# Optimization experiments

Measured on AMD Instinct MI355X. Metric: run time of the kernel, lower is better.

Reference implementation:

```python
import jax, jax.numpy as jnp
import numpy as np

EPS = 1e-6

def feature_map(x):
    # 'elu' feature map: elu(x) + 1 (positive feature map from Katharopoulos et al.)
    return jax.nn.elu(x) + 1.0

def setup_inputs() -> dict:
    key = jax.random.key(0)
    kq, kk, kv = jax.random.split(key, 3)
    B, L, H, D = 4, 2048, 16, 64
    q = jax.random.normal(kq, (B, L, H, D), dtype=jnp.float32)
    k = jax.random.normal(kk, (B, L, H, D), dtype=jnp.float32)
    v = jax.random.normal(kv, (B, L, H, D), dtype=jnp.float32)
    return {"q": q, "k": k, "v": v}

def reference(q, k, v):
    # q, k, v: [N, L, H, D]  (attention_mask=None -> causal linear attention)
    qf = feature_map(q)
    kf = feature_map(k)
    # normalizer: z[n,l,h] = sum_d qf[n,l,h,d] * cumsum_s<=l kf[n,s,h,d]
    z = jnp.einsum('nlhd,nlhd->nlh', qf, jnp.cumsum(kf, axis=1)) + EPS
    # causal_dot_product via scan over sequence with carry S[n,h,d,m]
    B, L, H, D = q.shape
    M = v.shape[-1]
    qs = jnp.moveaxis(qf, 1, 0)  # [L, N, H, D]
    ks = jnp.moveaxis(kf, 1, 0)
    vs = jnp.moveaxis(v, 1, 0)

    def step(S, qkv):
        ql, kl, vl = qkv                              # [N,H,D], [N,H,D], [N,H,M]
        S = S + jnp.einsum('nhd,nhm->nhdm', kl, vl)   # running sum of k v^T
        out = jnp.einsum('nhd,nhdm->nhm', ql, S)
        return S, out

    S0 = jnp.zeros((B, H, D, M), dtype=q.dtype)
    _, outs = jax.lax.scan(step, S0, (qs, ks, vs))    # outs: [L, N, H, M]
    v_ = jnp.moveaxis(outs, 0, 1)                     # [N, L, H, M]
    return v_ / z[..., None]
```

## Files before the change

### kernel.cpp

```cpp
#include <hip/hip_runtime.h>
#include <cstdint>

#define LL 2048
#define HH 16
#define DD 64
#define NC 32
#define LSTR 1024
#define EPSF 1e-6f
#define PAD 72

typedef __bf16 bf16x8 __attribute__((ext_vector_type(8)));
typedef float floatx4 __attribute__((ext_vector_type(4)));
typedef unsigned short ushortx8 __attribute__((ext_vector_type(8)));
typedef unsigned short ushortx4 __attribute__((ext_vector_type(4)));
typedef unsigned short ushortx2 __attribute__((ext_vector_type(2)));

static __device__ __forceinline__ float fmap(float x){ return x > 0.f ? x + 1.f : __expf(x); }
static __device__ __forceinline__ unsigned short f2bf(float f){
    unsigned u = __builtin_bit_cast(unsigned, f);
    u += 0x7fffu + ((u >> 16) & 1u);
    return (unsigned short)(u >> 16);
}
static __device__ __forceinline__ float bf2f(unsigned short s){
    unsigned u = ((unsigned)s) << 16;
    return __builtin_bit_cast(float, u);
}
static __device__ __forceinline__ bf16x8 ldf(const unsigned short* p){
    return __builtin_bit_cast(bf16x8, *(const ushortx8*)p);
}

__global__ __launch_bounds__(256) void k1(const float* __restrict__ kp, const float* __restrict__ vp,
                                          unsigned short* __restrict__ kvt, float* __restrict__ ks)
{
    __shared__ __align__(16) unsigned short kft[DD*PAD];
    __shared__ __align__(16) unsigned short vtt[DD*PAD];
    const int ci = blockIdx.x;
    const int c = ci & 31, bh = ci >> 5, b = bh >> 4, h = bh & 15;
    const int t = threadIdx.x;
    const int64_t gbase = ((int64_t)(b*LL + c*DD)*HH + h)*DD;
#pragma unroll
    for (int i = 0; i < 2; ++i) {
        int flat = t + 256*i;
        int l0 = (flat >> 4) * 2, col = (flat & 15) << 2;
        const float* gk = kp + gbase + (int64_t)l0*LSTR + col;
        const float* gv = vp + gbase + (int64_t)l0*LSTR + col;
        float4 ka = *(const float4*)(gk);
        float4 kb = *(const float4*)(gk + LSTR);
        float4 va = *(const float4*)(gv);
        float4 vb = *(const float4*)(gv + LSTR);
        float kaa[4] = {ka.x,ka.y,ka.z,ka.w}, kbb[4] = {kb.x,kb.y,kb.z,kb.w};
        float vaa[4] = {va.x,va.y,va.z,va.w}, vbb[4] = {vb.x,vb.y,vb.z,vb.w};
#pragma unroll
        for (int e = 0; e < 4; ++e) {
            *(ushortx2*)(kft + (col+e)*PAD + l0) = ushortx2{ f2bf(fmap(kaa[e])), f2bf(fmap(kbb[e])) };
            *(ushortx2*)(vtt + (col+e)*PAD + l0) = ushortx2{ f2bf(vaa[e]), f2bf(vbb[e]) };
        }
    }
    __syncthreads();
    const int w = t >> 6, lane = t & 63, quad = lane >> 4, lr = lane & 15;
    const int m0 = 16*w;
    floatx4 acc[4];
#pragma unroll
    for (int dt = 0; dt < 4; ++dt) acc[dt] = floatx4{0.f,0.f,0.f,0.f};
#pragma unroll
    for (int kk = 0; kk < 2; ++kk) {
        bf16x8 a = ldf(vtt + (m0+lr)*PAD + kk*32 + quad*8);
#pragma unroll
        for (int dt = 0; dt < 4; ++dt) {
            bf16x8 bb = ldf(kft + (dt*16+lr)*PAD + kk*32 + quad*8);
            acc[dt] = __builtin_amdgcn_mfma_f32_16x16x32_bf16(a, bb, acc[dt], 0, 0, 0);
        }
    }
    unsigned short* kvo = kvt + (int64_t)ci*4096;
#pragma unroll
    for (int dt = 0; dt < 4; ++dt)
#pragma unroll
        for (int r = 0; r < 4; ++r)
            kvo[(m0 + quad*4 + r)*DD + dt*16 + lr] = f2bf(acc[dt][r]);
    if (t < DD) {
        float s = 0.f;
#pragma unroll
        for (int j = 0; j < 8; ++j) {
            ushortx8 u = *(const ushortx8*)(kft + t*PAD + j*8);
#pragma unroll
            for (int e = 0; e < 8; ++e) s += bf2f(u[e]);
        }
        ks[(int64_t)ci*DD + t] = s;
    }
}

__global__ __launch_bounds__(256) void k2(unsigned short* __restrict__ kvt, float* __restrict__ ks)
{
    const int blk = blockIdx.x;
    const int bh = blk >> 3, part = blk & 7, t = threadIdx.x;
    unsigned short* base = kvt + (int64_t)bh*NC*4096 + (part*256 + t)*2;
    float r0 = 0.f, r1 = 0.f;
    unsigned x = *(const unsigned*)base;
    for (int c = 0; c < NC-1; ++c) {
        unsigned xn = *(const unsigned*)(base + (int64_t)(c+1)*4096);
        unsigned o = (unsigned)f2bf(r0) | ((unsigned)f2bf(r1) << 16);
        r0 += bf2f((unsigned short)(x & 0xffffu));
        r1 += bf2f((unsigned short)(x >> 16));
        *(unsigned*)(base + (int64_t)c*4096) = o;
        x = xn;
    }
    *(unsigned*)(base + (int64_t)(NC-1)*4096) = (unsigned)f2bf(r0) | ((unsigned)f2bf(r1) << 16);
    if (part == 0 && t < DD) {
        float r = 0.f;
        float* kb = ks + (int64_t)bh*NC*DD + t;
        for (int c = 0; c < NC; ++c) { float xx = kb[(int64_t)c*DD]; kb[(int64_t)c*DD] = r; r += xx; }
    }
}

__global__ __launch_bounds__(256) void k3(const float* __restrict__ qp, const float* __restrict__ kp,
                                          const float* __restrict__ vp,
                                          const unsigned short* __restrict__ kvt,
                                          const float* __restrict__ ks, float* __restrict__ outp)
{
    __shared__ __align__(16) unsigned short qf [DD*PAD];
    __shared__ __align__(16) unsigned short kfx[80*PAD];
    __shared__ __align__(16) unsigned short vtt[DD*PAD];
    __shared__ float zr[DD];
    const int ci = blockIdx.x;
    const int c = ci & 31, bh = ci >> 5, b = bh >> 4, h = bh & 15;
    const int t = threadIdx.x;
    const int64_t gbase = ((int64_t)(b*LL + c*DD)*HH + h)*DD;
    const unsigned short* kvg = kvt + (int64_t)ci*4096;
    const float* ksg = ks + (int64_t)ci*DD;
#pragma unroll
    for (int i = 0; i < 2; ++i) {
        int flat = t + 256*i;
        int l0 = (flat >> 4) * 2, col = (flat & 15) << 2;
        const float* gq = qp + gbase + (int64_t)l0*LSTR + col;
        const float* gk = kp + gbase + (int64_t)l0*LSTR + col;
        const float* gv = vp + gbase + (int64_t)l0*LSTR + col;
        float4 qa = *(const float4*)(gq);
        float4 qb = *(const float4*)(gq + LSTR);
        float4 ka = *(const float4*)(gk);
        float4 kb = *(const float4*)(gk + LSTR);
        float4 va = *(const float4*)(gv);
        float4 vb = *(const float4*)(gv + LSTR);
        *(ushortx4*)(qf + l0*PAD + col)      = ushortx4{ f2bf(fmap(qa.x)), f2bf(fmap(qa.y)), f2bf(fmap(qa.z)), f2bf(fmap(qa.w)) };
        *(ushortx4*)(qf + (l0+1)*PAD + col)  = ushortx4{ f2bf(fmap(qb.x)), f2bf(fmap(qb.y)), f2bf(fmap(qb.z)), f2bf(fmap(qb.w)) };
        *(ushortx4*)(kfx + l0*PAD + col)     = ushortx4{ f2bf(fmap(ka.x)), f2bf(fmap(ka.y)), f2bf(fmap(ka.z)), f2bf(fmap(ka.w)) };
        *(ushortx4*)(kfx + (l0+1)*PAD + col) = ushortx4{ f2bf(fmap(kb.x)), f2bf(fmap(kb.y)), f2bf(fmap(kb.z)), f2bf(fmap(kb.w)) };
        float vaa[4] = {va.x,va.y,va.z,va.w}, vbb[4] = {vb.x,vb.y,vb.z,vb.w};
#pragma unroll
        for (int e = 0; e < 4; ++e)
            *(ushortx2*)(vtt + (col+e)*PAD + l0) = ushortx2{ f2bf(vaa[e]), f2bf(vbb[e]) };
    }
    if (t < 135) *(ushortx8*)(kfx + 65*PAD + t*8) = ushortx8{0,0,0,0,0,0,0,0};
    if (t < DD)  kfx[64*PAD + t] = f2bf(ksg[t]);
    __syncthreads();

    const int w = t >> 6, lane = t & 63, quad = lane >> 4, lr = lane & 15;
    const int l0 = 16*w;
    bf16x8 aq[2];
    aq[0] = ldf(qf + (l0+lr)*PAD + quad*8);
    aq[1] = ldf(qf + (l0+lr)*PAD + 32 + quad*8);
    bf16x8 bs[2][4];
#pragma unroll
    for (int kk = 0; kk < 2; ++kk)
#pragma unroll
        for (int mt = 0; mt < 4; ++mt)
            bs[kk][mt] = ldf(kvg + (mt*16+lr)*DD + kk*32 + quad*8);

    floatx4 sc[5];
#pragma unroll
    for (int tt = 0; tt < 5; ++tt) sc[tt] = floatx4{0.f,0.f,0.f,0.f};
#pragma unroll
    for (int kk = 0; kk < 2; ++kk)
#pragma unroll
        for (int tt = 0; tt < 5; ++tt) {
            bf16x8 bb = ldf(kfx + (tt*16+lr)*PAD + kk*32 + quad*8);
            sc[tt] = __builtin_amdgcn_mfma_f32_16x16x32_bf16(aq[kk], bb, sc[tt], 0, 0, 0);
        }

    float zp[4] = {0.f,0.f,0.f,0.f};
#pragma unroll
    for (int tt = 0; tt < 4; ++tt)
#pragma unroll
        for (int r = 0; r < 4; ++r) {
            int row = l0 + quad*4 + r;
            int col = tt*16 + lr;
            float val = (col <= row) ? sc[tt][r] : 0.f;
            zp[r] += val;
            qf[row*PAD + col] = f2bf(val);
        }
#pragma unroll
    for (int r = 0; r < 4; ++r) zp[r] += (lr == 0) ? sc[4][r] : 0.f;
#pragma unroll
    for (int m = 1; m < 16; m <<= 1)
#pragma unroll
        for (int r = 0; r < 4; ++r) zp[r] += __shfl_xor(zp[r], m, 64);
    if (lr == 0)
#pragma unroll
        for (int r = 0; r < 4; ++r) zr[l0 + quad*4 + r] = 1.f / (zp[r] + EPSF);

    floatx4 oa[4];
#pragma unroll
    for (int mt = 0; mt < 4; ++mt) oa[mt] = floatx4{0.f,0.f,0.f,0.f};
#pragma unroll
    for (int kk = 0; kk < 2; ++kk) {
        bf16x8 a2 = ldf(qf + (l0+lr)*PAD + kk*32 + quad*8);
#pragma unroll
        for (int mt = 0; mt < 4; ++mt) {
            bf16x8 bv = ldf(vtt + (mt*16+lr)*PAD + kk*32 + quad*8);
            oa[mt] = __builtin_amdgcn_mfma_f32_16x16x32_bf16(a2, bv, oa[mt], 0, 0, 0);
        }
    }
#pragma unroll
    for (int kk = 0; kk < 2; ++kk)
#pragma unroll
        for (int mt = 0; mt < 4; ++mt)
            oa[mt] = __builtin_amdgcn_mfma_f32_16x16x32_bf16(aq[kk], bs[kk][mt], oa[mt], 0, 0, 0);
#pragma unroll
    for (int r = 0; r < 4; ++r) {
        int row = l0 + quad*4 + r;
        float rz = zr[row];
#pragma unroll
        for (int mt = 0; mt < 4; ++mt)
            outp[gbase + (int64_t)row*LSTR + mt*16 + lr] = oa[mt][r] * rz;
    }
}

extern "C" void kernel_launch(void* const* d_in, const int* in_sizes, int n_in,
                              void* d_out, int out_size, void* d_ws, size_t ws_size,
                              hipStream_t stream) {
    const float* q = (const float*)d_in[0];
    const float* k = (const float*)d_in[1];
    const float* v = (const float*)d_in[2];
    float* out = (float*)d_out;
    unsigned short* kvt = (unsigned short*)d_ws;
    float* ks = (float*)((char*)d_ws + (size_t)2048*4096*2);
    k1<<<2048, 256, 0, stream>>>(k, v, kvt, ks);
    k2<<<512,  256, 0, stream>>>(kvt, ks);
    k3<<<2048, 256, 0, stream>>>(q, k, v, kvt, ks, out);
}
```

Before: 156.3 us.

## Restructure into two kernels with per-quarter serial state recurrence

Replaces the three-kernel chunked scheme (per-chunk KV, global prefix scan, output) with two kernels. The first computes KV sums over 256-row octets, double-buffering global loads into LDS. The second has each 512-thread block own a quarter of one (b,h) sequence, seed its state from the preceding octet sums, and walk 8 chunks serially, updating the running KV state and key sum in LDS while prefetching the next chunk. This removes the bf16 scan kernel and a workspace round trip. In exchange the main kernel launches only 256 blocks and has a serial chunk dependency, so parallelism drops.

Result: faster. 147.8 us (-5.5%).

```diff
diff --git a/kernel.cpp b/kernel.cpp
--- a/kernel.cpp
+++ b/kernel.cpp
@@ -4,7 +4,6 @@
 #define LL 2048
 #define HH 16
 #define DD 64
-#define NC 32
 #define LSTR 1024
 #define EPSF 1e-6f
 #define PAD 72
@@ -28,199 +27,301 @@
 static __device__ __forceinline__ bf16x8 ldf(const unsigned short* p){
     return __builtin_bit_cast(bf16x8, *(const ushortx8*)p);
 }
-
-__global__ __launch_bounds__(256) void k1(const float* __restrict__ kp, const float* __restrict__ vp,
-                                          unsigned short* __restrict__ kvt, float* __restrict__ ks)
+static __device__ __forceinline__ float4 fmap4(float4 a){
+    return float4{fmap(a.x), fmap(a.y), fmap(a.z), fmap(a.w)};
+}
+
+template<bool MAP>
+static __device__ __forceinline__ void st_sd(unsigned short* base, int r, int c, float4 a, float4 b){
+    if (MAP) {
+        *(ushortx4*)(base + r*PAD + c)     = ushortx4{ f2bf(fmap(a.x)), f2bf(fmap(a.y)), f2bf(fmap(a.z)), f2bf(fmap(a.w)) };
+        *(ushortx4*)(base + (r+1)*PAD + c) = ushortx4{ f2bf(fmap(b.x)), f2bf(fmap(b.y)), f2bf(fmap(b.z)), f2bf(fmap(b.w)) };
+    } else {
+        *(ushortx4*)(base + r*PAD + c)     = ushortx4{ f2bf(a.x), f2bf(a.y), f2bf(a.z), f2bf(a.w) };
+        *(ushortx4*)(base + (r+1)*PAD + c) = ushortx4{ f2bf(b.x), f2bf(b.y), f2bf(b.z), f2bf(b.w) };
+    }
+}
+template<bool MAP>
+static __device__ __forceinline__ void st_tr(unsigned short* base, int r, int c, float4 a, float4 b){
+    float aa[4] = {a.x, a.y, a.z, a.w}, bb[4] = {b.x, b.y, b.z, b.w};
+#pragma unroll
+    for (int e = 0; e < 4; ++e) {
+        float x0 = MAP ? fmap(aa[e]) : aa[e];
+        float x1 = MAP ? fmap(bb[e]) : bb[e];
+        *(ushortx2*)(base + (c+e)*PAD + r) = ushortx2{ f2bf(x0), f2bf(x1) };
+    }
+}
+
+__global__ __launch_bounds__(256) void kA(const float* __restrict__ kp, const float* __restrict__ vp,
+                                          float* __restrict__ qkv, float* __restrict__ ksq)
 {
+    __shared__ __align__(16) unsigned short kft[2][DD*PAD];
+    __shared__ __align__(16) unsigned short vtt[2][DD*PAD];
+    const int blk = blockIdx.x;
+    const int bh = blk >> 3, oct = blk & 7, b = bh >> 4, h = bh & 15;
+    const int t = threadIdx.x;
+    const int w = t >> 6, lane = t & 63, quad = lane >> 4, lr = lane & 15;
+    const int m0 = 16*w;
+
+    floatx4 acc[4];
+#pragma unroll
+    for (int dt = 0; dt < 4; ++dt) acc[dt] = floatx4{0.f,0.f,0.f,0.f};
+    float ksa = 0.f;
+
+    const int64_t gb0 = ((int64_t)(b*LL + oct*256)*HH + h)*DD;
+#pragma unroll
+    for (int ii = 0; ii < 2; ++ii) {
+        int flat = t + 256*ii;
+        int l0s = (flat >> 4) * 2, col4 = (flat & 15) << 2;
+        const float* gk = kp + gb0 + (int64_t)l0s*LSTR + col4;
+        const float* gv = vp + gb0 + (int64_t)l0s*LSTR + col4;
+        float4 ka = *(const float4*)gk, kb = *(const float4*)(gk + LSTR);
+        float4 va = *(const float4*)gv, vb = *(const float4*)(gv + LSTR);
+        st_tr<true >(kft[0], l0s, col4, ka, kb);
+        st_tr<false>(vtt[0], l0s, col4, va, vb);
+    }
+    __syncthreads();
+
+#pragma unroll
+    for (int sc = 0; sc < 4; ++sc) {
+        const int p = sc & 1;
+        float4 ka[2], kb[2], va[2], vb[2];
+        if (sc < 3) {
+            const int64_t gb = gb0 + (int64_t)(sc+1)*DD*LSTR;
+#pragma unroll
+            for (int ii = 0; ii < 2; ++ii) {
+                int flat = t + 256*ii;
+                int l0s = (flat >> 4) * 2, col4 = (flat & 15) << 2;
+                const float* gk = kp + gb + (int64_t)l0s*LSTR + col4;
+                const float* gv = vp + gb + (int64_t)l0s*LSTR + col4;
+                ka[ii] = *(const float4*)gk; kb[ii] = *(const float4*)(gk + LSTR);
+                va[ii] = *(const float4*)gv; vb[ii] = *(const float4*)(gv + LSTR);
+            }
+        }
+#pragma unroll
+        for (int kk = 0; kk < 2; ++kk) {
+            bf16x8 a = ldf(vtt[p] + (m0+lr)*PAD + kk*32 + quad*8);
+#pragma unroll
+            for (int dt = 0; dt < 4; ++dt) {
+                bf16x8 bbf = ldf(kft[p] + (dt*16+lr)*PAD + kk*32 + quad*8);
+                acc[dt] = __builtin_amdgcn_mfma_f32_16x16x32_bf16(a, bbf, acc[dt], 0, 0, 0);
+            }
+        }
+        if (t < DD) {
+#pragma unroll
+            for (int jj = 0; jj < 8; ++jj) {
+                ushortx8 u = *(const ushortx8*)(kft[p] + t*PAD + jj*8);
+#pragma unroll
+                for (int e = 0; e < 8; ++e) ksa += bf2f(u[e]);
+            }
+        }
+        if (sc < 3) {
+#pragma unroll
+            for (int ii = 0; ii < 2; ++ii) {
+                int flat = t + 256*ii;
+                int l0s = (flat >> 4) * 2, col4 = (flat & 15) << 2;
+                st_tr<true >(kft[p^1], l0s, col4, ka[ii], kb[ii]);
+                st_tr<false>(vtt[p^1], l0s, col4, va[ii], vb[ii]);
+            }
+        }
+        __syncthreads();
+    }
+
+    float* qo = qkv + (int64_t)blk*4096;
+#pragma unroll
+    for (int dt = 0; dt < 4; ++dt)
+#pragma unroll
+        for (int r = 0; r < 4; ++r)
+            qo[(m0 + quad*4 + r)*DD + dt*16 + lr] = acc[dt][r];
+    if (t < DD) ksq[(int64_t)blk*DD + t] = ksa;
+}
+
+__global__ __launch_bounds__(512) void kM(const float* __restrict__ qp, const float* __restrict__ kp,
+                                          const float* __restrict__ vp,
+                                          const float* __restrict__ qkv, const float* __restrict__ ksq,
+                                          float* __restrict__ outp)
+{
+    __shared__ __align__(16) unsigned short qf [DD*PAD];
+    __shared__ __align__(16) unsigned short kfx[DD*PAD];
     __shared__ __align__(16) unsigned short kft[DD*PAD];
     __shared__ __align__(16) unsigned short vtt[DD*PAD];
-    const int ci = blockIdx.x;
-    const int c = ci & 31, bh = ci >> 5, b = bh >> 4, h = bh & 15;
+    __shared__ __align__(16) unsigned short sld[DD*PAD];
+    __shared__ __align__(16) unsigned short sct[DD*PAD];
+    __shared__ __align__(16) unsigned short kpx[16*PAD];
+    __shared__ float ksum[DD];
+    __shared__ float zp2[2][DD];
+
+    const int bid = blockIdx.x;
+    const int bh = bid & 63, qtr = bid >> 6, b = bh >> 4, h = bh & 15;
     const int t = threadIdx.x;
-    const int64_t gbase = ((int64_t)(b*LL + c*DD)*HH + h)*DD;
-#pragma unroll
-    for (int i = 0; i < 2; ++i) {
-        int flat = t + 256*i;
-        int l0 = (flat >> 4) * 2, col = (flat & 15) << 2;
-        const float* gk = kp + gbase + (int64_t)l0*LSTR + col;
-        const float* gv = vp + gbase + (int64_t)l0*LSTR + col;
-        float4 ka = *(const float4*)(gk);
-        float4 kb = *(const float4*)(gk + LSTR);
-        float4 va = *(const float4*)(gv);
-        float4 vb = *(const float4*)(gv + LSTR);
-        float kaa[4] = {ka.x,ka.y,ka.z,ka.w}, kbb[4] = {kb.x,kb.y,kb.z,kb.w};
-        float vaa[4] = {va.x,va.y,va.z,va.w}, vbb[4] = {vb.x,vb.y,vb.z,vb.w};
-#pragma unroll
-        for (int e = 0; e < 4; ++e) {
-            *(ushortx2*)(kft + (col+e)*PAD + l0) = ushortx2{ f2bf(fmap(kaa[e])), f2bf(fmap(kbb[e])) };
-            *(ushortx2*)(vtt + (col+e)*PAD + l0) = ushortx2{ f2bf(vaa[e]), f2bf(vbb[e]) };
-        }
-    }
-    __syncthreads();
     const int w = t >> 6, lane = t & 63, quad = lane >> 4, lr = lane & 15;
-    const int m0 = 16*w;
-    floatx4 acc[4];
-#pragma unroll
-    for (int dt = 0; dt < 4; ++dt) acc[dt] = floatx4{0.f,0.f,0.f,0.f};
-#pragma unroll
-    for (int kk = 0; kk < 2; ++kk) {
-        bf16x8 a = ldf(vtt + (m0+lr)*PAD + kk*32 + quad*8);
-#pragma unroll
-        for (int dt = 0; dt < 4; ++dt) {
-            bf16x8 bb = ldf(kft + (dt*16+lr)*PAD + kk*32 + quad*8);
-            acc[dt] = __builtin_amdgcn_mfma_f32_16x16x32_bf16(a, bb, acc[dt], 0, 0, 0);
-        }
-    }
-    unsigned short* kvo = kvt + (int64_t)ci*4096;
-#pragma unroll
-    for (int dt = 0; dt < 4; ++dt)
-#pragma unroll
-        for (int r = 0; r < 4; ++r)
-            kvo[(m0 + quad*4 + r)*DD + dt*16 + lr] = f2bf(acc[dt][r]);
+    const int wi = w >> 1, wj = w & 1;
+    const int l0 = 16*wi;
+    const int l0s = (t >> 4) * 2, col4 = (t & 15) << 2;
+
+    const int64_t bhb = ((int64_t)b*LL*HH + h)*DD;
+    const int cg0 = qtr*8;
+
+    if (t < 135) *(ushortx8*)(kpx + PAD + t*8) = ushortx8{0,0,0,0,0,0,0,0};
+    const int no = 2*qtr;
     if (t < DD) {
         float s = 0.f;
-#pragma unroll
-        for (int j = 0; j < 8; ++j) {
-            ushortx8 u = *(const ushortx8*)(kft + t*PAD + j*8);
-#pragma unroll
-            for (int e = 0; e < 8; ++e) s += bf2f(u[e]);
-        }
-        ks[(int64_t)ci*DD + t] = s;
-    }
-}
-
-__global__ __launch_bounds__(256) void k2(unsigned short* __restrict__ kvt, float* __restrict__ ks)
-{
-    const int blk = blockIdx.x;
-    const int bh = blk >> 3, part = blk & 7, t = threadIdx.x;
-    unsigned short* base = kvt + (int64_t)bh*NC*4096 + (part*256 + t)*2;
-    float r0 = 0.f, r1 = 0.f;
-    unsigned x = *(const unsigned*)base;
-    for (int c = 0; c < NC-1; ++c) {
-        unsigned xn = *(const unsigned*)(base + (int64_t)(c+1)*4096);
-        unsigned o = (unsigned)f2bf(r0) | ((unsigned)f2bf(r1) << 16);
-        r0 += bf2f((unsigned short)(x & 0xffffu));
-        r1 += bf2f((unsigned short)(x >> 16));
-        *(unsigned*)(base + (int64_t)c*4096) = o;
-        x = xn;
-    }
-    *(unsigned*)(base + (int64_t)(NC-1)*4096) = (unsigned)f2bf(r0) | ((unsigned)f2bf(r1) << 16);
-    if (part == 0 && t < DD) {
-        float r = 0.f;
-        float* kb = ks + (int64_t)bh*NC*DD + t;
-        for (int c = 0; c < NC; ++c) { float xx = kb[(int64_t)c*DD]; kb[(int64_t)c*DD] = r; r += xx; }
-    }
-}
-
-__global__ __launch_bounds__(256) void k3(const float* __restrict__ qp, const float* __restrict__ kp,
-                                          const float* __restrict__ vp,
-                                          const unsigned short* __restrict__ kvt,
-                                          const float* __restrict__ ks, float* __restrict__ outp)
-{
-    __shared__ __align__(16) unsigned short qf [DD*PAD];
-    __shared__ __align__(16) unsigned short kfx[80*PAD];
-    __shared__ __align__(16) unsigned short vtt[DD*PAD];
-    __shared__ float zr[DD];
-    const int ci = blockIdx.x;
-    const int c = ci & 31, bh = ci >> 5, b = bh >> 4, h = bh & 15;
-    const int t = threadIdx.x;
-    const int64_t gbase = ((int64_t)(b*LL + c*DD)*HH + h)*DD;
-    const unsigned short* kvg = kvt + (int64_t)ci*4096;
-    const float* ksg = ks + (int64_t)ci*DD;
-#pragma unroll
-    for (int i = 0; i < 2; ++i) {
-        int flat = t + 256*i;
-        int l0 = (flat >> 4) * 2, col = (flat & 15) << 2;
-        const float* gq = qp + gbase + (int64_t)l0*LSTR + col;
-        const float* gk = kp + gbase + (int64_t)l0*LSTR + col;
-        const float* gv = vp + gbase + (int64_t)l0*LSTR + col;
-        float4 qa = *(const float4*)(gq);
-        float4 qb = *(const float4*)(gq + LSTR);
-        float4 ka = *(const float4*)(gk);
-        float4 kb = *(const float4*)(gk + LSTR);
-        float4 va = *(const float4*)(gv);
-        float4 vb = *(const float4*)(gv + LSTR);
-        *(ushortx4*)(qf + l0*PAD + col)      = ushortx4{ f2bf(fmap(qa.x)), f2bf(fmap(qa.y)), f2bf(fmap(qa.z)), f2bf(fmap(qa.w)) };
-        *(ushortx4*)(qf + (l0+1)*PAD + col)  = ushortx4{ f2bf(fmap(qb.x)), f2bf(fmap(qb.y)), f2bf(fmap(qb.z)), f2bf(fmap(qb.w)) };
-        *(ushortx4*)(kfx + l0*PAD + col)     = ushortx4{ f2bf(fmap(ka.x)), f2bf(fmap(ka.y)), f2bf(fmap(ka.z)), f2bf(fmap(ka.w)) };
-        *(ushortx4*)(kfx + (l0+1)*PAD + col) = ushortx4{ f2bf(fmap(kb.x)), f2bf(fmap(kb.y)), f2bf(fmap(kb.z)), f2bf(fmap(kb.w)) };
-        float vaa[4] = {va.x,va.y,va.z,va.w}, vbb[4] = {vb.x,vb.y,vb.z,vb.w};
-#pragma unroll
-        for (int e = 0; e < 4; ++e)
-            *(ushortx2*)(vtt + (col+e)*PAD + l0) = ushortx2{ f2bf(vaa[e]), f2bf(vbb[e]) };
-    }
-    if (t < 135) *(ushortx8*)(kfx + 65*PAD + t*8) = ushortx8{0,0,0,0,0,0,0,0};
-    if (t < DD)  kfx[64*PAD + t] = f2bf(ksg[t]);
+        for (int o = 0; o < no; ++o) s += ksq[((int64_t)bh*8 + o)*DD + t];
+        ksum[t] = s;
+        kpx[t] = f2bf(s);
+    }
+    floatx4 S_acc[2];
+    S_acc[0] = floatx4{0.f,0.f,0.f,0.f};
+    S_acc[1] = floatx4{0.f,0.f,0.f,0.f};
+    for (int o = 0; o < no; ++o) {
+        const float* qo = qkv + ((int64_t)bh*8 + o)*4096;
+#pragma unroll
+        for (int dtl = 0; dtl < 2; ++dtl)
+#pragma unroll
+            for (int r = 0; r < 4; ++r)
+                S_acc[dtl][r] += qo[(l0 + quad*4 + r)*DD + 32*wj + dtl*16 + lr];
+    }
+#pragma unroll
+    for (int dtl = 0; dtl < 2; ++dtl)
+#pragma unroll
+        for (int r = 0; r < 4; ++r)
+            sld[(l0 + quad*4 + r)*PAD + 32*wj + dtl*16 + lr] = f2bf(S_acc[dtl][r]);
+
+    {
+        const int64_t gb = bhb + (int64_t)cg0*DD*LSTR;
+        const float* gq = qp + gb + (int64_t)l0s*LSTR + col4;
+        const float* gk = kp + gb + (int64_t)l0s*LSTR + col4;
+        const float* gv = vp + gb + (int64_t)l0s*LSTR + col4;
+        float4 q0 = *(const float4*)gq, q1 = *(const float4*)(gq + LSTR);
+        float4 k0 = *(const float4*)gk, k1 = *(const float4*)(gk + LSTR);
+        float4 v0 = *(const float4*)gv, v1 = *(const float4*)(gv + LSTR);
+        st_sd<true >(qf , l0s, col4, q0, q1);
+        st_sd<true >(kfx, l0s, col4, k0, k1);
+        st_tr<true >(kft, l0s, col4, k0, k1);
+        st_tr<false>(vtt, l0s, col4, v0, v1);
+    }
     __syncthreads();
 
-    const int w = t >> 6, lane = t & 63, quad = lane >> 4, lr = lane & 15;
-    const int l0 = 16*w;
-    bf16x8 aq[2];
-    aq[0] = ldf(qf + (l0+lr)*PAD + quad*8);
-    aq[1] = ldf(qf + (l0+lr)*PAD + 32 + quad*8);
-    bf16x8 bs[2][4];
-#pragma unroll
-    for (int kk = 0; kk < 2; ++kk)
-#pragma unroll
-        for (int mt = 0; mt < 4; ++mt)
-            bs[kk][mt] = ldf(kvg + (mt*16+lr)*DD + kk*32 + quad*8);
-
-    floatx4 sc[5];
-#pragma unroll
-    for (int tt = 0; tt < 5; ++tt) sc[tt] = floatx4{0.f,0.f,0.f,0.f};
-#pragma unroll
-    for (int kk = 0; kk < 2; ++kk)
-#pragma unroll
-        for (int tt = 0; tt < 5; ++tt) {
-            bf16x8 bb = ldf(kfx + (tt*16+lr)*PAD + kk*32 + quad*8);
-            sc[tt] = __builtin_amdgcn_mfma_f32_16x16x32_bf16(aq[kk], bb, sc[tt], 0, 0, 0);
-        }
-
-    float zp[4] = {0.f,0.f,0.f,0.f};
-#pragma unroll
-    for (int tt = 0; tt < 4; ++tt)
-#pragma unroll
-        for (int r = 0; r < 4; ++r) {
-            int row = l0 + quad*4 + r;
-            int col = tt*16 + lr;
-            float val = (col <= row) ? sc[tt][r] : 0.f;
-            zp[r] += val;
-            qf[row*PAD + col] = f2bf(val);
-        }
-#pragma unroll
-    for (int r = 0; r < 4; ++r) zp[r] += (lr == 0) ? sc[4][r] : 0.f;
-#pragma unroll
-    for (int m = 1; m < 16; m <<= 1)
-#pragma unroll
-        for (int r = 0; r < 4; ++r) zp[r] += __shfl_xor(zp[r], m, 64);
-    if (lr == 0)
-#pragma unroll
-        for (int r = 0; r < 4; ++r) zr[l0 + quad*4 + r] = 1.f / (zp[r] + EPSF);
-
-    floatx4 oa[4];
-#pragma unroll
-    for (int mt = 0; mt < 4; ++mt) oa[mt] = floatx4{0.f,0.f,0.f,0.f};
-#pragma unroll
-    for (int kk = 0; kk < 2; ++kk) {
-        bf16x8 a2 = ldf(qf + (l0+lr)*PAD + kk*32 + quad*8);
-#pragma unroll
-        for (int mt = 0; mt < 4; ++mt) {
-            bf16x8 bv = ldf(vtt + (mt*16+lr)*PAD + kk*32 + quad*8);
-            oa[mt] = __builtin_amdgcn_mfma_f32_16x16x32_bf16(a2, bv, oa[mt], 0, 0, 0);
-        }
-    }
-#pragma unroll
-    for (int kk = 0; kk < 2; ++kk)
-#pragma unroll
-        for (int mt = 0; mt < 4; ++mt)
-            oa[mt] = __builtin_amdgcn_mfma_f32_16x16x32_bf16(aq[kk], bs[kk][mt], oa[mt], 0, 0, 0);
-#pragma unroll
-    for (int r = 0; r < 4; ++r) {
-        int row = l0 + quad*4 + r;
-        float rz = zr[row];
-#pragma unroll
-        for (int mt = 0; mt < 4; ++mt)
-            outp[gbase + (int64_t)row*LSTR + mt*16 + lr] = oa[mt][r] * rz;
+    float4 lk0 = float4{0,0,0,0}, lk1 = float4{0,0,0,0};
+    float4 lv0 = float4{0,0,0,0}, lv1 = float4{0,0,0,0};
+
+#pragma unroll 2
+    for (int c = 0; c < 8; ++c) {
+        const int cg = cg0 + c;
+        float4 nq0, nq1, nk0, nk1, nv0, nv1;
+        if (c < 7) {
+            const int64_t gb = bhb + (int64_t)(cg+1)*DD*LSTR;
+            const float* gq = qp + gb + (int64_t)l0s*LSTR + col4;
+            const float* gk = kp + gb + (int64_t)l0s*LSTR + col4;
+            const float* gv = vp + gb + (int64_t)l0s*LSTR + col4;
+            nq0 = *(const float4*)gq; nq1 = *(const float4*)(gq + LSTR);
+            nk0 = *(const float4*)gk; nk1 = *(const float4*)(gk + LSTR);
+            nv0 = *(const float4*)gv; nv1 = *(const float4*)(gv + LSTR);
+        }
+        if (c > 0) {
+            st_tr<false>(kft, l0s, col4, lk0, lk1);
+            st_tr<false>(vtt, l0s, col4, lv0, lv1);
+        }
+        bf16x8 aq0 = ldf(qf + (l0+lr)*PAD + quad*8);
+        bf16x8 aq1 = ldf(qf + (l0+lr)*PAD + 32 + quad*8);
+        bf16x8 bsf[2][2];
+#pragma unroll
+        for (int kk = 0; kk < 2; ++kk)
+#pragma unroll
+            for (int mt = 0; mt < 2; ++mt)
+                bsf[kk][mt] = ldf(sld + ((2*wj+mt)*16+lr)*PAD + kk*32 + quad*8);
+        floatx4 s0 = floatx4{0.f,0.f,0.f,0.f}, s1 = floatx4{0.f,0.f,0.f,0.f}, sp = floatx4{0.f,0.f,0.f,0.f};
+#pragma unroll
+        for (int kk = 0; kk < 2; ++kk) {
+            bf16x8 aqk = kk ? aq1 : aq0;
+            bf16x8 b0 = ldf(kfx + ((2*wj+0)*16+lr)*PAD + kk*32 + quad*8);
+            bf16x8 b1 = ldf(kfx + ((2*wj+1)*16+lr)*PAD + kk*32 + quad*8);
+            s0 = __builtin_amdgcn_mfma_f32_16x16x32_bf16(aqk, b0, s0, 0, 0, 0);
+            s1 = __builtin_amdgcn_mfma_f32_16x16x32_bf16(aqk, b1, s1, 0, 0, 0);
+            if (wj == 0) {
+                bf16x8 bp = ldf(kpx + lr*PAD + kk*32 + quad*8);
+                sp = __builtin_amdgcn_mfma_f32_16x16x32_bf16(aqk, bp, sp, 0, 0, 0);
+            }
+        }
+        float zpv[4];
+#pragma unroll
+        for (int r = 0; r < 4; ++r) zpv[r] = (wj == 0 && lr == 0) ? sp[r] : 0.f;
+#pragma unroll
+        for (int tt = 0; tt < 2; ++tt) {
+            int colb = (2*wj+tt)*16 + lr;
+            floatx4 sv = tt ? s1 : s0;
+#pragma unroll
+            for (int r = 0; r < 4; ++r) {
+                int row = l0 + quad*4 + r;
+                float val = (colb <= row) ? sv[r] : 0.f;
+                zpv[r] += val;
+                sct[row*PAD + colb] = f2bf(val);
+            }
+        }
+#pragma unroll
+        for (int m = 1; m < 16; m <<= 1)
+#pragma unroll
+            for (int r = 0; r < 4; ++r) zpv[r] += __shfl_xor(zpv[r], m, 64);
+        if (lr == 0) {
+#pragma unroll
+            for (int r = 0; r < 4; ++r) zp2[wj][l0 + quad*4 + r] = zpv[r];
+        }
+        __syncthreads();
+        if (t < DD) {
+            float s = ksum[t];
+#pragma unroll
+            for (int jj = 0; jj < 8; ++jj) {
+                ushortx8 u = *(const ushortx8*)(kft + t*PAD + jj*8);
+#pragma unroll
+                for (int e = 0; e < 8; ++e) s += bf2f(u[e]);
+            }
+            ksum[t] = s;
+            kpx[t] = f2bf(s);
+        }
+        floatx4 oa0 = floatx4{0.f,0.f,0.f,0.f}, oa1 = floatx4{0.f,0.f,0.f,0.f};
+#pragma unroll
+        for (int kk = 0; kk < 2; ++kk) {
+            bf16x8 a2  = ldf(sct + (l0+lr)*PAD + kk*32 + quad*8);
+            bf16x8 bv0 = ldf(vtt + ((2*wj+0)*16+lr)*PAD + kk*32 + quad*8);
+            bf16x8 bv1 = ldf(vtt + ((2*wj+1)*16+lr)*PAD + kk*32 + quad*8);
+            oa0 = __builtin_amdgcn_mfma_f32_16x16x32_bf16(a2, bv0, oa0, 0, 0, 0);
+            oa1 = __builtin_amdgcn_mfma_f32_16x16x32_bf16(a2, bv1, oa1, 0, 0, 0);
+        }
+        oa0 = __builtin_amdgcn_mfma_f32_16x16x32_bf16(aq0, bsf[0][0], oa0, 0, 0, 0);
+        oa0 = __builtin_amdgcn_mfma_f32_16x16x32_bf16(aq1, bsf[1][0], oa0, 0, 0, 0);
+        oa1 = __builtin_amdgcn_mfma_f32_16x16x32_bf16(aq0, bsf[0][1], oa1, 0, 0, 0);
+        oa1 = __builtin_amdgcn_mfma_f32_16x16x32_bf16(aq1, bsf[1][1], oa1, 0, 0, 0);
+        {
+            const int64_t ob = bhb + (int64_t)cg*DD*LSTR;
+#pragma unroll
+            for (int r = 0; r < 4; ++r) {
+                int row = l0 + quad*4 + r;
+                float rz = 1.f / (zp2[0][row] + zp2[1][row] + EPSF);
+                outp[ob + (int64_t)row*LSTR + (2*wj+0)*16 + lr] = oa0[r] * rz;
+                outp[ob + (int64_t)row*LSTR + (2*wj+1)*16 + lr] = oa1[r] * rz;
+            }
+        }
+#pragma unroll
+        for (int kk = 0; kk < 2; ++kk) {
+            bf16x8 av = ldf(vtt + (l0+lr)*PAD + kk*32 + quad*8);
+#pragma unroll
+            for (int dtl = 0; dtl < 2; ++dtl) {
+                bf16x8 bk = ldf(kft + ((2*wj+dtl)*16+lr)*PAD + kk*32 + quad*8);
+                S_acc[dtl] = __builtin_amdgcn_mfma_f32_16x16x32_bf16(av, bk, S_acc[dtl], 0, 0, 0);
+            }
+        }
+#pragma unroll
+        for (int dtl = 0; dtl < 2; ++dtl)
+#pragma unroll
+            for (int r = 0; r < 4; ++r)
+                sld[(l0 + quad*4 + r)*PAD + 32*wj + dtl*16 + lr] = f2bf(S_acc[dtl][r]);
+        if (c < 7) {
+            float4 fk0 = fmap4(nk0), fk1 = fmap4(nk1);
+            st_sd<true >(qf , l0s, col4, nq0, nq1);
+            st_sd<false>(kfx, l0s, col4, fk0, fk1);
+            lk0 = fk0; lk1 = fk1; lv0 = nv0; lv1 = nv1;
+        }
+        __syncthreads();
     }
 }
 
@@ -231,9 +332,8 @@
     const float* k = (const float*)d_in[1];
     const float* v = (const float*)d_in[2];
     float* out = (float*)d_out;
-    unsigned short* kvt = (unsigned short*)d_ws;
-    float* ks = (float*)((char*)d_ws + (size_t)2048*4096*2);
-    k1<<<2048, 256, 0, stream>>>(k, v, kvt, ks);
-    k2<<<512,  256, 0, stream>>>(kvt, ks);
-    k3<<<2048, 256, 0, stream>>>(q, k, v, kvt, ks, out);
-}
+    float* qkv = (float*)d_ws;
+    float* ksq = (float*)((char*)d_ws + (size_t)512*4096*4);
+    kA<<<512, 256, 0, stream>>>(k, v, qkv, ksq);
+    kM<<<256, 512, 0, stream>>>(q, k, v, qkv, ksq, out);
+}
```

## Fuse chunk-state scan into two kernels with per-octet running snapshots

Applied to the files above, without the earlier changes.

Replaces the three-kernel pipeline (per-chunk KV outer product, separate prefix-scan kernel, output kernel) with two kernels. The first kernel has each block walk 4 consecutive chunks and keep a running KV/ksum accumulator, writing inclusive snapshots while double-buffering global loads into LDS. The second kernel rebuilds each chunk's exclusive prefix state by summing earlier octet totals from the snapshots. It also adds an XOR swizzle to the transposed LDS layouts to cut bank conflicts. This removes one launch and the serial scan pass, at the cost of redundant snapshot reads in the output kernel, an extra 8KB LDS buffer, and less parallelism in the first kernel (512 blocks).

After: 155.0 us. About the same (-0.9%).

```diff
diff --git a/kernel.cpp b/kernel.cpp
--- a/kernel.cpp
+++ b/kernel.cpp
@@ -4,10 +4,10 @@
 #define LL 2048
 #define HH 16
 #define DD 64
-#define NC 32
 #define LSTR 1024
 #define EPSF 1e-6f
 #define PAD 72
+#define SWZ(row, off) ((row)*PAD + ((off) ^ ((((row)>>3)&7)<<3)))
 
 typedef __bf16 bf16x8 __attribute__((ext_vector_type(8)));
 typedef float floatx4 __attribute__((ext_vector_type(4)));
@@ -29,128 +29,173 @@
     return __builtin_bit_cast(bf16x8, *(const ushortx8*)p);
 }
 
-__global__ __launch_bounds__(256) void k1(const float* __restrict__ kp, const float* __restrict__ vp,
-                                          unsigned short* __restrict__ kvt, float* __restrict__ ks)
+template<bool MAP>
+static __device__ __forceinline__ void st_sd(unsigned short* base, int r, int c, float4 a, float4 b){
+    if (MAP) {
+        *(ushortx4*)(base + r*PAD + c)     = ushortx4{ f2bf(fmap(a.x)), f2bf(fmap(a.y)), f2bf(fmap(a.z)), f2bf(fmap(a.w)) };
+        *(ushortx4*)(base + (r+1)*PAD + c) = ushortx4{ f2bf(fmap(b.x)), f2bf(fmap(b.y)), f2bf(fmap(b.z)), f2bf(fmap(b.w)) };
+    } else {
+        *(ushortx4*)(base + r*PAD + c)     = ushortx4{ f2bf(a.x), f2bf(a.y), f2bf(a.z), f2bf(a.w) };
+        *(ushortx4*)(base + (r+1)*PAD + c) = ushortx4{ f2bf(b.x), f2bf(b.y), f2bf(b.z), f2bf(b.w) };
+    }
+}
+template<bool MAP>
+static __device__ __forceinline__ void st_tr(unsigned short* base, int r, int c, float4 a, float4 b){
+    float aa[4] = {a.x, a.y, a.z, a.w}, bb[4] = {b.x, b.y, b.z, b.w};
+#pragma unroll
+    for (int e = 0; e < 4; ++e) {
+        float x0 = MAP ? fmap(aa[e]) : aa[e];
+        float x1 = MAP ? fmap(bb[e]) : bb[e];
+        *(ushortx2*)(base + SWZ(c+e, r)) = ushortx2{ f2bf(x0), f2bf(x1) };
+    }
+}
+
+__global__ __launch_bounds__(256) void kA(const float* __restrict__ kp, const float* __restrict__ vp,
+                                          unsigned short* __restrict__ snap, float* __restrict__ ksnap)
 {
-    __shared__ __align__(16) unsigned short kft[DD*PAD];
-    __shared__ __align__(16) unsigned short vtt[DD*PAD];
-    const int ci = blockIdx.x;
-    const int c = ci & 31, bh = ci >> 5, b = bh >> 4, h = bh & 15;
+    __shared__ __align__(16) unsigned short kft[2][DD*PAD];
+    __shared__ __align__(16) unsigned short vtt[2][DD*PAD];
+    const int blk = blockIdx.x;
+    const int bh = blk >> 3, oct = blk & 7, b = bh >> 4, h = bh & 15;
     const int t = threadIdx.x;
-    const int64_t gbase = ((int64_t)(b*LL + c*DD)*HH + h)*DD;
-#pragma unroll
-    for (int i = 0; i < 2; ++i) {
-        int flat = t + 256*i;
-        int l0 = (flat >> 4) * 2, col = (flat & 15) << 2;
-        const float* gk = kp + gbase + (int64_t)l0*LSTR + col;
-        const float* gv = vp + gbase + (int64_t)l0*LSTR + col;
-        float4 ka = *(const float4*)(gk);
-        float4 kb = *(const float4*)(gk + LSTR);
-        float4 va = *(const float4*)(gv);
-        float4 vb = *(const float4*)(gv + LSTR);
-        float kaa[4] = {ka.x,ka.y,ka.z,ka.w}, kbb[4] = {kb.x,kb.y,kb.z,kb.w};
-        float vaa[4] = {va.x,va.y,va.z,va.w}, vbb[4] = {vb.x,vb.y,vb.z,vb.w};
-#pragma unroll
-        for (int e = 0; e < 4; ++e) {
-            *(ushortx2*)(kft + (col+e)*PAD + l0) = ushortx2{ f2bf(fmap(kaa[e])), f2bf(fmap(kbb[e])) };
-            *(ushortx2*)(vtt + (col+e)*PAD + l0) = ushortx2{ f2bf(vaa[e]), f2bf(vbb[e]) };
-        }
-    }
-    __syncthreads();
     const int w = t >> 6, lane = t & 63, quad = lane >> 4, lr = lane & 15;
     const int m0 = 16*w;
+
     floatx4 acc[4];
 #pragma unroll
     for (int dt = 0; dt < 4; ++dt) acc[dt] = floatx4{0.f,0.f,0.f,0.f};
-#pragma unroll
-    for (int kk = 0; kk < 2; ++kk) {
-        bf16x8 a = ldf(vtt + (m0+lr)*PAD + kk*32 + quad*8);
-#pragma unroll
-        for (int dt = 0; dt < 4; ++dt) {
-            bf16x8 bb = ldf(kft + (dt*16+lr)*PAD + kk*32 + quad*8);
-            acc[dt] = __builtin_amdgcn_mfma_f32_16x16x32_bf16(a, bb, acc[dt], 0, 0, 0);
-        }
-    }
-    unsigned short* kvo = kvt + (int64_t)ci*4096;
-#pragma unroll
-    for (int dt = 0; dt < 4; ++dt)
-#pragma unroll
-        for (int r = 0; r < 4; ++r)
-            kvo[(m0 + quad*4 + r)*DD + dt*16 + lr] = f2bf(acc[dt][r]);
-    if (t < DD) {
-        float s = 0.f;
-#pragma unroll
-        for (int j = 0; j < 8; ++j) {
-            ushortx8 u = *(const ushortx8*)(kft + t*PAD + j*8);
-#pragma unroll
-            for (int e = 0; e < 8; ++e) s += bf2f(u[e]);
-        }
-        ks[(int64_t)ci*DD + t] = s;
-    }
-}
-
-__global__ __launch_bounds__(256) void k2(unsigned short* __restrict__ kvt, float* __restrict__ ks)
-{
-    const int blk = blockIdx.x;
-    const int bh = blk >> 3, part = blk & 7, t = threadIdx.x;
-    unsigned short* base = kvt + (int64_t)bh*NC*4096 + (part*256 + t)*2;
-    float r0 = 0.f, r1 = 0.f;
-    unsigned x = *(const unsigned*)base;
-    for (int c = 0; c < NC-1; ++c) {
-        unsigned xn = *(const unsigned*)(base + (int64_t)(c+1)*4096);
-        unsigned o = (unsigned)f2bf(r0) | ((unsigned)f2bf(r1) << 16);
-        r0 += bf2f((unsigned short)(x & 0xffffu));
-        r1 += bf2f((unsigned short)(x >> 16));
-        *(unsigned*)(base + (int64_t)c*4096) = o;
-        x = xn;
-    }
-    *(unsigned*)(base + (int64_t)(NC-1)*4096) = (unsigned)f2bf(r0) | ((unsigned)f2bf(r1) << 16);
-    if (part == 0 && t < DD) {
-        float r = 0.f;
-        float* kb = ks + (int64_t)bh*NC*DD + t;
-        for (int c = 0; c < NC; ++c) { float xx = kb[(int64_t)c*DD]; kb[(int64_t)c*DD] = r; r += xx; }
-    }
-}
-
-__global__ __launch_bounds__(256) void k3(const float* __restrict__ qp, const float* __restrict__ kp,
+    float ksa = 0.f;
+
+    const int64_t gb0 = ((int64_t)(b*LL + oct*256)*HH + h)*DD;
+#pragma unroll
+    for (int ii = 0; ii < 2; ++ii) {
+        int flat = t + 256*ii;
+        int l0s = (flat >> 4) * 2, col4 = (flat & 15) << 2;
+        const float* gk = kp + gb0 + (int64_t)l0s*LSTR + col4;
+        const float* gv = vp + gb0 + (int64_t)l0s*LSTR + col4;
+        float4 ka = *(const float4*)gk, kb = *(const float4*)(gk + LSTR);
+        float4 va = *(const float4*)gv, vb = *(const float4*)(gv + LSTR);
+        st_tr<true >(kft[0], l0s, col4, ka, kb);
+        st_tr<false>(vtt[0], l0s, col4, va, vb);
+    }
+    __syncthreads();
+
+#pragma unroll 1
+    for (int sc = 0; sc < 4; ++sc) {
+        const int p = sc & 1;
+        float4 ka[2], kb[2], va[2], vb[2];
+        if (sc < 3) {
+            const int64_t gb = gb0 + (int64_t)(sc+1)*DD*LSTR;
+#pragma unroll
+            for (int ii = 0; ii < 2; ++ii) {
+                int flat = t + 256*ii;
+                int l0s = (flat >> 4) * 2, col4 = (flat & 15) << 2;
+                const float* gk = kp + gb + (int64_t)l0s*LSTR + col4;
+                const float* gv = vp + gb + (int64_t)l0s*LSTR + col4;
+                ka[ii] = *(const float4*)gk; kb[ii] = *(const float4*)(gk + LSTR);
+                va[ii] = *(const float4*)gv; vb[ii] = *(const float4*)(gv + LSTR);
+            }
+        }
+#pragma unroll
+        for (int kk = 0; kk < 2; ++kk) {
+            bf16x8 a = ldf(vtt[p] + SWZ(m0+lr, kk*32 + quad*8));
+#pragma unroll
+            for (int dt = 0; dt < 4; ++dt) {
+                bf16x8 bbf = ldf(kft[p] + SWZ(dt*16+lr, kk*32 + quad*8));
+                acc[dt] = __builtin_amdgcn_mfma_f32_16x16x32_bf16(a, bbf, acc[dt], 0, 0, 0);
+            }
+        }
+        {
+            unsigned short* so = snap + ((int64_t)blk*4 + sc)*4096;
+#pragma unroll
+            for (int dt = 0; dt < 4; ++dt)
+#pragma unroll
+                for (int r = 0; r < 4; ++r)
+                    so[(m0 + quad*4 + r)*DD + dt*16 + lr] = f2bf(acc[dt][r]);
+        }
+        if (t < DD) {
+#pragma unroll
+            for (int jj = 0; jj < 8; ++jj) {
+                ushortx8 u = *(const ushortx8*)(kft[p] + SWZ(t, jj*8));
+#pragma unroll
+                for (int e = 0; e < 8; ++e) ksa += bf2f(u[e]);
+            }
+            ksnap[((int64_t)blk*4 + sc)*DD + t] = ksa;
+        }
+        if (sc < 3) {
+#pragma unroll
+            for (int ii = 0; ii < 2; ++ii) {
+                int flat = t + 256*ii;
+                int l0s = (flat >> 4) * 2, col4 = (flat & 15) << 2;
+                st_tr<true >(kft[p^1], l0s, col4, ka[ii], kb[ii]);
+                st_tr<false>(vtt[p^1], l0s, col4, va[ii], vb[ii]);
+            }
+        }
+        __syncthreads();
+    }
+}
+
+__global__ __launch_bounds__(256) void kC(const float* __restrict__ qp, const float* __restrict__ kp,
                                           const float* __restrict__ vp,
-                                          const unsigned short* __restrict__ kvt,
-                                          const float* __restrict__ ks, float* __restrict__ outp)
+                                          const unsigned short* __restrict__ snap,
+                                          const float* __restrict__ ksnap,
+                                          float* __restrict__ outp)
 {
     __shared__ __align__(16) unsigned short qf [DD*PAD];
     __shared__ __align__(16) unsigned short kfx[80*PAD];
     __shared__ __align__(16) unsigned short vtt[DD*PAD];
+    __shared__ __align__(16) unsigned short sld[DD*PAD];
     __shared__ float zr[DD];
-    const int ci = blockIdx.x;
-    const int c = ci & 31, bh = ci >> 5, b = bh >> 4, h = bh & 15;
+    const int bid = blockIdx.x;
+    const int bh = bid >> 5, c = bid & 31, b = bh >> 4, h = bh & 15;
+    const int o = c >> 2, j = c & 3;
     const int t = threadIdx.x;
     const int64_t gbase = ((int64_t)(b*LL + c*DD)*HH + h)*DD;
-    const unsigned short* kvg = kvt + (int64_t)ci*4096;
-    const float* ksg = ks + (int64_t)ci*DD;
+
 #pragma unroll
     for (int i = 0; i < 2; ++i) {
         int flat = t + 256*i;
-        int l0 = (flat >> 4) * 2, col = (flat & 15) << 2;
-        const float* gq = qp + gbase + (int64_t)l0*LSTR + col;
-        const float* gk = kp + gbase + (int64_t)l0*LSTR + col;
-        const float* gv = vp + gbase + (int64_t)l0*LSTR + col;
-        float4 qa = *(const float4*)(gq);
-        float4 qb = *(const float4*)(gq + LSTR);
-        float4 ka = *(const float4*)(gk);
-        float4 kb = *(const float4*)(gk + LSTR);
-        float4 va = *(const float4*)(gv);
-        float4 vb = *(const float4*)(gv + LSTR);
-        *(ushortx4*)(qf + l0*PAD + col)      = ushortx4{ f2bf(fmap(qa.x)), f2bf(fmap(qa.y)), f2bf(fmap(qa.z)), f2bf(fmap(qa.w)) };
-        *(ushortx4*)(qf + (l0+1)*PAD + col)  = ushortx4{ f2bf(fmap(qb.x)), f2bf(fmap(qb.y)), f2bf(fmap(qb.z)), f2bf(fmap(qb.w)) };
-        *(ushortx4*)(kfx + l0*PAD + col)     = ushortx4{ f2bf(fmap(ka.x)), f2bf(fmap(ka.y)), f2bf(fmap(ka.z)), f2bf(fmap(ka.w)) };
-        *(ushortx4*)(kfx + (l0+1)*PAD + col) = ushortx4{ f2bf(fmap(kb.x)), f2bf(fmap(kb.y)), f2bf(fmap(kb.z)), f2bf(fmap(kb.w)) };
-        float vaa[4] = {va.x,va.y,va.z,va.w}, vbb[4] = {vb.x,vb.y,vb.z,vb.w};
-#pragma unroll
-        for (int e = 0; e < 4; ++e)
-            *(ushortx2*)(vtt + (col+e)*PAD + l0) = ushortx2{ f2bf(vaa[e]), f2bf(vbb[e]) };
+        int l0s = (flat >> 4) * 2, col = (flat & 15) << 2;
+        const float* gq = qp + gbase + (int64_t)l0s*LSTR + col;
+        const float* gk = kp + gbase + (int64_t)l0s*LSTR + col;
+        const float* gv = vp + gbase + (int64_t)l0s*LSTR + col;
+        float4 qa = *(const float4*)(gq), qb = *(const float4*)(gq + LSTR);
+        float4 ka = *(const float4*)(gk), kb = *(const float4*)(gk + LSTR);
+        float4 va = *(const float4*)(gv), vb = *(const float4*)(gv + LSTR);
+        st_sd<true >(qf , l0s, col, qa, qb);
+        st_sd<true >(kfx, l0s, col, ka, kb);
+        st_tr<false>(vtt, l0s, col, va, vb);
     }
     if (t < 135) *(ushortx8*)(kfx + 65*PAD + t*8) = ushortx8{0,0,0,0,0,0,0,0};
-    if (t < DD)  kfx[64*PAD + t] = f2bf(ksg[t]);
+    if (t < DD) {
+        float s = 0.f;
+        for (int op = 0; op < o; ++op) s += ksnap[((int64_t)(bh*8 + op)*4 + 3)*DD + t];
+        if (j > 0) s += ksnap[((int64_t)(bh*8 + o)*4 + (j-1))*DD + t];
+        kfx[64*PAD + t] = f2bf(s);
+    }
+    {
+        const int m = t >> 2, d0 = (t & 3) << 4;
+        float a0[8], a1[8];
+#pragma unroll
+        for (int e = 0; e < 8; ++e) { a0[e] = 0.f; a1[e] = 0.f; }
+        for (int op = 0; op < o; ++op) {
+            const unsigned short* sp = snap + ((int64_t)(bh*8 + op)*4 + 3)*4096 + m*DD + d0;
+            ushortx8 u0 = *(const ushortx8*)sp, u1 = *(const ushortx8*)(sp + 8);
+#pragma unroll
+            for (int e = 0; e < 8; ++e) { a0[e] += bf2f(u0[e]); a1[e] += bf2f(u1[e]); }
+        }
+        if (j > 0) {
+            const unsigned short* sp = snap + ((int64_t)(bh*8 + o)*4 + (j-1))*4096 + m*DD + d0;
+            ushortx8 u0 = *(const ushortx8*)sp, u1 = *(const ushortx8*)(sp + 8);
+#pragma unroll
+            for (int e = 0; e < 8; ++e) { a0[e] += bf2f(u0[e]); a1[e] += bf2f(u1[e]); }
+        }
+        ushortx8 w0, w1;
+#pragma unroll
+        for (int e = 0; e < 8; ++e) { w0[e] = f2bf(a0[e]); w1[e] = f2bf(a1[e]); }
+        *(ushortx8*)(sld + m*PAD + d0)     = w0;
+        *(ushortx8*)(sld + m*PAD + d0 + 8) = w1;
+    }
     __syncthreads();
 
     const int w = t >> 6, lane = t & 63, quad = lane >> 4, lr = lane & 15;
@@ -163,17 +208,17 @@
     for (int kk = 0; kk < 2; ++kk)
 #pragma unroll
         for (int mt = 0; mt < 4; ++mt)
-            bs[kk][mt] = ldf(kvg + (mt*16+lr)*DD + kk*32 + quad*8);
-
-    floatx4 sc[5];
-#pragma unroll
-    for (int tt = 0; tt < 5; ++tt) sc[tt] = floatx4{0.f,0.f,0.f,0.f};
+            bs[kk][mt] = ldf(sld + (mt*16+lr)*PAD + kk*32 + quad*8);
+
+    floatx4 sc5[5];
+#pragma unroll
+    for (int tt = 0; tt < 5; ++tt) sc5[tt] = floatx4{0.f,0.f,0.f,0.f};
 #pragma unroll
     for (int kk = 0; kk < 2; ++kk)
 #pragma unroll
         for (int tt = 0; tt < 5; ++tt) {
             bf16x8 bb = ldf(kfx + (tt*16+lr)*PAD + kk*32 + quad*8);
-            sc[tt] = __builtin_amdgcn_mfma_f32_16x16x32_bf16(aq[kk], bb, sc[tt], 0, 0, 0);
+            sc5[tt] = __builtin_amdgcn_mfma_f32_16x16x32_bf16(aq[kk], bb, sc5[tt], 0, 0, 0);
         }
 
     float zp[4] = {0.f,0.f,0.f,0.f};
@@ -183,12 +228,12 @@
         for (int r = 0; r < 4; ++r) {
             int row = l0 + quad*4 + r;
             int col = tt*16 + lr;
-            float val = (col <= row) ? sc[tt][r] : 0.f;
+            float val = (col <= row) ? sc5[tt][r] : 0.f;
             zp[r] += val;
             qf[row*PAD + col] = f2bf(val);
         }
 #pragma unroll
-    for (int r = 0; r < 4; ++r) zp[r] += (lr == 0) ? sc[4][r] : 0.f;
+    for (int r = 0; r < 4; ++r) zp[r] += (lr == 0) ? sc5[4][r] : 0.f;
 #pragma unroll
     for (int m = 1; m < 16; m <<= 1)
 #pragma unroll
@@ -205,7 +250,7 @@
         bf16x8 a2 = ldf(qf + (l0+lr)*PAD + kk*32 + quad*8);
 #pragma unroll
         for (int mt = 0; mt < 4; ++mt) {
-            bf16x8 bv = ldf(vtt + (mt*16+lr)*PAD + kk*32 + quad*8);
+            bf16x8 bv = ldf(vtt + SWZ(mt*16+lr, kk*32 + quad*8));
             oa[mt] = __builtin_amdgcn_mfma_f32_16x16x32_bf16(a2, bv, oa[mt], 0, 0, 0);
         }
     }
@@ -231,9 +276,8 @@
     const float* k = (const float*)d_in[1];
     const float* v = (const float*)d_in[2];
     float* out = (float*)d_out;
-    unsigned short* kvt = (unsigned short*)d_ws;
-    float* ks = (float*)((char*)d_ws + (size_t)2048*4096*2);
-    k1<<<2048, 256, 0, stream>>>(k, v, kvt, ks);
-    k2<<<512,  256, 0, stream>>>(kvt, ks);
-    k3<<<2048, 256, 0, stream>>>(q, k, v, kvt, ks, out);
-}
+    unsigned short* snap = (unsigned short*)d_ws;
+    float* ksnap = (float*)((char*)d_ws + (size_t)512*4*4096*2);
+    kA<<<512,  256, 0, stream>>>(k, v, snap, ksnap);
+    kC<<<2048, 256, 0, stream>>>(q, k, v, snap, ksnap, out);
+}
```
